# Performance work log

Measured on AMD Instinct MI355X. Metric: run time of the kernel, lower is better.

Reference implementation:

```python
import jax, jax.numpy as jnp
import numpy as np

NS, NV = 32, 8                      # scalar / vector multiplicities (32x0e + 8x1o)
N_NODES, N_EDGES = 16384, 131072
NEF, HID = 128, 128                 # edge feature dim, MLP hidden
WN = NS*NS + NV*NS + NS*NV + NV*NV  # 1600 tensor-product weights per edge
D = NS + 3*NV                       # 56 node feature dim
INV_SQRT3 = 1.0/np.sqrt(3.0)        # CG coeff for 1o x 1o -> 0e
PATH_NORM = 1.0/np.sqrt(NS + NV)    # fan-in normalization per output irrep
EPS = 1e-5


def setup_inputs() -> dict:
    key = jax.random.key(0)
    ks = jax.random.split(key, 10)
    node_attr = jax.random.normal(ks[0], (N_NODES, D), jnp.float32)
    edge_index = jax.random.randint(ks[1], (2, N_EDGES), 0, N_NODES, dtype=jnp.int64)
    edge_attr = jax.random.normal(ks[2], (N_EDGES, NEF), jnp.float32)
    edge_sh = jax.random.normal(ks[3], (N_EDGES, 4), jnp.float32)
    W1 = jax.random.normal(ks[4], (NEF, HID), jnp.float32) / np.sqrt(NEF)
    b1 = jnp.zeros((HID,), jnp.float32)
    W2 = jax.random.normal(ks[5], (HID, WN), jnp.float32) / np.sqrt(HID)
    b2 = jnp.zeros((WN,), jnp.float32)
    bn_gamma = jnp.ones((NS + NV,), jnp.float32)   # per-irrep scale (scalars then vectors)
    bn_beta = jnp.zeros((NS,), jnp.float32)        # bias only on scalar irreps
    return dict(node_attr=node_attr, edge_attr=edge_attr, edge_sh=edge_sh,
                W1=W1, b1=b1, W2=W2, b2=b2, bn_gamma=bn_gamma, bn_beta=bn_beta,
                edge_index=edge_index)


def reference(node_attr, edge_attr, edge_sh, W1, b1, W2, b2, bn_gamma, bn_beta, edge_index):
    edge_src, edge_dst = edge_index[0], edge_index[1]

    # per-edge tensor-product weights from edge MLP (dropout=0, eval mode)
    w = jax.nn.relu(edge_attr @ W1 + b1) @ W2 + b2            # [E, WN]
    o0 = NS*NS; o1 = o0 + NV*NS; o2 = o1 + NS*NV
    w_ss = w[:, :o0].reshape(-1, NS, NS)   # 0e x 0e -> 0e
    w_vs = w[:, o0:o1].reshape(-1, NV, NS) # 1o x 1o -> 0e
    w_sv = w[:, o1:o2].reshape(-1, NS, NV) # 0e x 1o -> 1o
    w_vv = w[:, o2:].reshape(-1, NV, NV)   # 1o x 0e -> 1o

    # gather node features onto edges
    x = node_attr[edge_dst]                # [E, D]
    xs = x[:, :NS]                         # [E, NS]
    xv = x[:, NS:].reshape(-1, NV, 3)      # [E, NV, 3]
    ss = edge_sh[:, 0]                     # [E]
    sv = edge_sh[:, 1:4]                   # [E, 3]

    # CG tensor product with per-edge fully-connected weights
    dot_vv = jnp.einsum('eim,em->ei', xv, sv) * INV_SQRT3
    out_s = (jnp.einsum('eij,ei->ej', w_ss, xs) * ss[:, None]
             + jnp.einsum('eij,ei->ej', w_vs, dot_vv)) * PATH_NORM          # [E, NS]
    out_v = (jnp.einsum('eij,ei->ej', w_sv, xs)[:, :, None] * sv[:, None, :]
             + jnp.einsum('eij,eim->ejm', w_vv, xv) * ss[:, None, None]) * PATH_NORM  # [E, NV, 3]
    tp = jnp.concatenate([out_s, out_v.reshape(-1, 3*NV)], axis=-1)         # [E, D]

    # scatter-mean to source nodes
    sums = jax.ops.segment_sum(tp, edge_src, num_segments=N_NODES)
    cnt = jax.ops.segment_sum(jnp.ones((tp.shape[0], 1), tp.dtype), edge_src,
                              num_segments=N_NODES)
    out = sums / jnp.maximum(cnt, 1.0)

    # residual (in/out irreps identical -> zero padding is a no-op)
    out = out + node_attr

    # equivariant batch norm (training-mode batch statistics)
    s = out[:, :NS]
    v = out[:, NS:].reshape(-1, NV, 3)
    s = (s - s.mean(0)) / jnp.sqrt(s.var(0) + EPS) * bn_gamma[:NS] + bn_beta
    vn2 = (v * v).sum(-1).mean(0)                               # [NV] mean squared norm
    v = v / jnp.sqrt(vn2 + EPS)[None, :, None] * bn_gamma[NS:][None, :, None]
    return jnp.concatenate([s, v.reshape(-1, 3*NV)], axis=-1)
```

## Files before the change

kernel.cpp:

```cpp
#include <hip/hip_runtime.h>

typedef short short8 __attribute__((ext_vector_type(8)));
typedef unsigned short us4 __attribute__((ext_vector_type(4)));
typedef float floatx4 __attribute__((ext_vector_type(4)));
typedef unsigned short u16;

#define NN 16384
#define NE 131072
#define NEF_ 128
#define DD 56
#define INV_SQRT3F 0.57735026918962576f
#define PATH_NORMF 0.15811388300841897f

__device__ __forceinline__ float bf2f(u16 u) {
    union { unsigned int i; float f; } v; v.i = ((unsigned int)u) << 16; return v.f;
}
__device__ __forceinline__ u16 f2bf(float f) {
    union { float f; unsigned int i; } v; v.f = f;
    unsigned int r = v.i + 0x7fffu + ((v.i >> 16) & 1u);
    return (u16)(r >> 16);
}

__global__ __launch_bounds__(256) void prep(const float* __restrict__ W1,
                                            const float* __restrict__ W2,
                                            u16* __restrict__ W1f,
                                            u16* __restrict__ W2f,
                                            const int* __restrict__ eidx,
                                            int* __restrict__ deg) {
    int b = blockIdx.x;
    if (b < 864) {
        int i = b * 256 + threadIdx.x;
        if (i < 16384) {
            int cc = i >> 13, kk = (i >> 11) & 3, cg = (i >> 9) & 3;
            int lane = (i >> 3) & 63, j = i & 7;
            int q = lane >> 4, m = lane & 15;
            W1f[i] = f2bf(W1[(kk * 32 + q * 8 + j) * 128 + cc * 64 + cg * 16 + m]);
        } else {
            int f = i - 16384;
            int c = f >> 13, kk = (f >> 11) & 3, cg = (f >> 9) & 3;
            int lane = (f >> 3) & 63, j = f & 7;
            int q = lane >> 4, m = lane & 15;
            W2f[f] = f2bf(W2[(kk * 32 + q * 8 + j) * 1600 + c * 64 + cg * 16 + m]);
        }
    } else {
        int e = (b - 864) * 256 + threadIdx.x;
        atomicAdd(&deg[eidx[e]], 1);
    }
}

__global__ __launch_bounds__(1024) void deg_scan(const int* __restrict__ deg,
                                                 int* __restrict__ row_start,
                                                 int* __restrict__ cursor) {
    __shared__ int part[1024];
    const int t = threadIdx.x;
    const int base = t * 16;
    int loc[16];
    int s = 0;
    #pragma unroll
    for (int i = 0; i < 16; i++) { loc[i] = s; s += deg[base + i]; }
    part[t] = s;
    __syncthreads();
    for (int off = 1; off < 1024; off <<= 1) {
        int v = (t >= off) ? part[t - off] : 0;
        __syncthreads();
        part[t] += v;
        __syncthreads();
    }
    int pre = (t == 0) ? 0 : part[t - 1];
    #pragma unroll
    for (int i = 0; i < 16; i++) {
        int v = pre + loc[i];
        row_start[base + i] = v;
        cursor[base + i] = v;
    }
    if (t == 1023) row_start[16384] = pre + s;
}

__global__ __launch_bounds__(256) void edge_scatter(const int* __restrict__ eidx,
                                                    int* __restrict__ cursor,
                                                    int* __restrict__ edge_order) {
    int e = blockIdx.x * 256 + threadIdx.x;
    int p = atomicAdd(&cursor[eidx[e]], 1);
    edge_order[p] = e;
}

__global__ __launch_bounds__(256, 2) void tpconv(
    const float* __restrict__ node_attr, const float* __restrict__ edge_attr,
    const float* __restrict__ edge_sh, const u16* __restrict__ W1f,
    const float* __restrict__ b1, const u16* __restrict__ W2f,
    const float* __restrict__ b2, const int* __restrict__ eidx,
    const int* __restrict__ edge_order,
    float* __restrict__ tp)
{
    __shared__ __align__(16) char smem[42496];
    u16*   sA  = (u16*)smem;
    u16*   sF  = (u16*)(smem + 17408);
    float* b2s = (float*)(smem + 26112);
    float* Ssc  = (float*)smem;
    float* Svec = (float*)(smem + 16896);

    const int t = threadIdx.x;
    const int lane = t & 63;
    const int cg = t >> 6;
    const int m = lane & 15;
    const int q = lane >> 4;
    const int p0 = blockIdx.x * 64;

    short8 fc[4];
    #pragma unroll
    for (int kk = 0; kk < 4; kk++)
        fc[kk] = *(const short8*)&W2f[(kk * 4 + cg) * 512 + lane * 8];

    for (int i = t; i < 1600; i += 256) b2s[i] = b2[i];

    #pragma unroll
    for (int ii = 0; ii < 8; ii++) {
        int cid = t + 256 * ii;
        int r = cid >> 5, s = cid & 31;
        int e = edge_order[p0 + r];
        const float* src = &edge_attr[(size_t)e * NEF_ + s * 4];
        us4 o;
        o.x = f2bf(src[0]); o.y = f2bf(src[1]); o.z = f2bf(src[2]); o.w = f2bf(src[3]);
        *(us4*)&sA[r * 136 + s * 4] = o;
    }
    {
        int e = t & 63, p = t >> 6;
        int eg = edge_order[p0 + e];
        int nd = eidx[NE + eg];
        const float* na = node_attr + (size_t)nd * DD;
        const float* sh = edge_sh + (size_t)eg * 4;
        if (p < 2) {
            #pragma unroll
            for (int k = 0; k < 16; k++)
                sF[(p * 16 + k) * 64 + e] = f2bf(na[p * 16 + k]);
        } else {
            #pragma unroll
            for (int k = 0; k < 12; k++)
                sF[(40 + (p - 2) * 12 + k) * 64 + e] = f2bf(na[32 + (p - 2) * 12 + k]);
        }
        sF[(64 + p) * 64 + e] = f2bf(sh[p]);
        float s0 = sh[1], s1 = sh[2], s2 = sh[3];
        #pragma unroll
        for (int s = 0; s < 2; s++) {
            int i = p + 4 * s;
            float d = (na[32 + 3 * i] * s0 + na[33 + 3 * i] * s1 + na[34 + 3 * i] * s2) * INV_SQRT3F;
            sF[(32 + i) * 64 + e] = f2bf(d);
        }
    }
    __syncthreads();

    floatx4 hacc[2][4];
    #pragma unroll
    for (int cc = 0; cc < 2; cc++) {
        short8 g[4];
        #pragma unroll
        for (int kk = 0; kk < 4; kk++)
            g[kk] = *(const short8*)&W1f[cc * 8192 + (kk * 4 + cg) * 512 + lane * 8];
        float bv = b1[cc * 64 + cg * 16 + m];
        #pragma unroll
        for (int et = 0; et < 4; et++) hacc[cc][et] = (floatx4){bv, bv, bv, bv};
        #pragma unroll
        for (int kk = 0; kk < 4; kk++)
            #pragma unroll
            for (int et = 0; et < 4; et++) {
                short8 a = *(const short8*)&sA[(et * 16 + m) * 136 + kk * 32 + q * 8];
                hacc[cc][et] = __builtin_amdgcn_mfma_f32_16x16x32_bf16(a, g[kk], hacc[cc][et], 0, 0, 0);
            }
    }
    __syncthreads();
    #pragma unroll
    for (int cc = 0; cc < 2; cc++)
      #pragma unroll
      for (int et = 0; et < 4; et++)
        #pragma unroll
        for (int r = 0; r < 4; r++) {
            int e = et * 16 + q * 4 + r;
            float v = hacc[cc][et][r];
            sA[e * 136 + cc * 64 + cg * 16 + m] = f2bf(v > 0.f ? v : 0.f);
        }
    __syncthreads();

    short8 hc[4][4];
    #pragma unroll
    for (int et = 0; et < 4; et++)
        #pragma unroll
        for (int kk = 0; kk < 4; kk++)
            hc[et][kk] = *(const short8*)&sA[(et * 16 + m) * 136 + kk * 32 + q * 8];

    float ssc[4], svc[4][3];
    #pragma unroll
    for (int et = 0; et < 4; et++) {
        ssc[et]    = bf2f(sF[64 * 64 + et * 16 + m]);
        svc[et][0] = bf2f(sF[65 * 64 + et * 16 + m]);
        svc[et][1] = bf2f(sF[66 * 64 + et * 16 + m]);
        svc[et][2] = bf2f(sF[67 * 64 + et * 16 + m]);
    }

    float tps[4][4];
    float tpv[4][4][3];
    #pragma unroll
    for (int et = 0; et < 4; et++)
        #pragma unroll
        for (int r = 0; r < 4; r++) {
            tps[et][r] = 0.f;
            tpv[et][r][0] = 0.f; tpv[et][r][1] = 0.f; tpv[et][r][2] = 0.f;
        }

    short8 fn[4];
    for (int c = 0; c < 25; c++) {
        if (c < 24) {
            #pragma unroll
            for (int kk = 0; kk < 4; kk++)
                fn[kk] = *(const short8*)&W2f[(size_t)(c + 1) * 8192 + (kk * 4 + cg) * 512 + lane * 8];
        }
        floatx4 bias = *(const floatx4*)&b2s[c * 64 + cg * 16 + q * 4];
        floatx4 acc[4];
        #pragma unroll
        for (int et = 0; et < 4; et++) acc[et] = bias;
        #pragma unroll
        for (int kk = 0; kk < 4; kk++)
            #pragma unroll
            for (int et = 0; et < 4; et++)
                acc[et] = __builtin_amdgcn_mfma_f32_16x16x32_bf16(fc[kk], hc[et][kk], acc[et], 0, 0, 0);

        if (c < 16) {
            const int i = 2 * c + (cg >> 1);
            #pragma unroll
            for (int et = 0; et < 4; et++) {
                float f = bf2f(sF[i * 64 + et * 16 + m]) * ssc[et];
                #pragma unroll
                for (int r = 0; r < 4; r++) tps[et][r] += acc[et][r] * f;
            }
        } else if (c < 20) {
            const int i = 2 * (c - 16) + (cg >> 1);
            #pragma unroll
            for (int et = 0; et < 4; et++) {
                float f = bf2f(sF[(32 + i) * 64 + et * 16 + m]);
                #pragma unroll
                for (int r = 0; r < 4; r++) tps[et][r] += acc[et][r] * f;
            }
        } else if (c < 24) {
            const int i = 8 * (c - 20) + cg * 2 + (q >> 1);
            #pragma unroll
            for (int et = 0; et < 4; et++) {
                float f = bf2f(sF[i * 64 + et * 16 + m]);
                #pragma unroll
                for (int r = 0; r < 4; r++) {
                    float t0 = acc[et][r] * f;
                    tpv[et][r][0] += t0 * svc[et][0];
                    tpv[et][r][1] += t0 * svc[et][1];
                    tpv[et][r][2] += t0 * svc[et][2];
                }
            }
        } else {
            const int i = cg * 2 + (q >> 1);
            #pragma unroll
            for (int et = 0; et < 4; et++) {
                float x0 = bf2f(sF[(40 + 3 * i + 0) * 64 + et * 16 + m]) * ssc[et];
                float x1 = bf2f(sF[(40 + 3 * i + 1) * 64 + et * 16 + m]) * ssc[et];
                float x2 = bf2f(sF[(40 + 3 * i + 2) * 64 + et * 16 + m]) * ssc[et];
                #pragma unroll
                for (int r = 0; r < 4; r++) {
                    tpv[et][r][0] += acc[et][r] * x0;
                    tpv[et][r][1] += acc[et][r] * x1;
                    tpv[et][r][2] += acc[et][r] * x2;
                }
            }
        }

        if (c < 24) {
            #pragma unroll
            for (int kk = 0; kk < 4; kk++) fc[kk] = fn[kk];
        }
    }

    __syncthreads();
    #pragma unroll
    for (int et = 0; et < 4; et++)
        #pragma unroll
        for (int r = 0; r < 4; r++)
            Ssc[(cg >> 1) * 2112 + (et * 16 + m) * 33 + (cg & 1) * 16 + q * 4 + r] = tps[et][r];
    #pragma unroll
    for (int et = 0; et < 4; et++)
        #pragma unroll
        for (int r = 0; r < 4; r++)
            #pragma unroll
            for (int mm = 0; mm < 3; mm++) {
                float v = tpv[et][r][mm];
                v += __shfl_xor(v, 32, 64);
                if (q < 2)
                    Svec[cg * 1600 + (et * 16 + m) * 25 + ((q & 1) * 4 + r) * 3 + mm] = v;
            }
    __syncthreads();

    for (int idx = t; idx < 3584; idx += 256) {
        int e = idx / 56, d = idx - e * 56;
        float v;
        if (d < 32) {
            v = Ssc[e * 33 + d] + Ssc[2112 + e * 33 + d];
        } else {
            int dd = d - 32;
            v = Svec[e * 25 + dd] + Svec[1600 + e * 25 + dd]
              + Svec[3200 + e * 25 + dd] + Svec[4800 + e * 25 + dd];
        }
        tp[(size_t)(p0 + e) * DD + d] = v * PATH_NORMF;
    }
}

__global__ __launch_bounds__(256) void gather_finalize(
    const float* __restrict__ tp, const int* __restrict__ row_start,
    const float* __restrict__ node_attr,
    float* __restrict__ ybuf, float* __restrict__ partial)
{
    __shared__ float ps[4][72];
    const int wv = threadIdx.x >> 6, lane = threadIdx.x & 63;
    const int n = blockIdx.x * 4 + wv;
    const int beg = row_start[n], end = row_start[n + 1];
    if (lane < 56) {
        float acc = 0.f;
        for (int p = beg; p < end; p++)
            acc += tp[(size_t)p * DD + lane];
        float inv = 1.f / fmaxf((float)(end - beg), 1.f);
        float y = acc * inv + node_attr[(size_t)n * DD + lane];
        ybuf[(size_t)n * DD + lane] = y;
        if (lane < 32) {
            ps[wv][lane] = y;
            ps[wv][32 + lane] = y * y;
        } else {
            float vv = y * y;
            float v1 = __shfl_down(vv, 1, 64);
            float v2 = __shfl_down(vv, 2, 64);
            int l3 = lane - 32;
            if (l3 % 3 == 0) ps[wv][64 + l3 / 3] = vv + v1 + v2;
        }
    }
    __syncthreads();
    const int t = threadIdx.x;
    if (t < 72)
        partial[(size_t)blockIdx.x * 72 + t] = ps[0][t] + ps[1][t] + ps[2][t] + ps[3][t];
}

__global__ __launch_bounds__(256) void bn_reduce(const float* __restrict__ partial,
                                                 float* __restrict__ stats)
{
    __shared__ float red[256];
    const int d = blockIdx.x;
    const int t = threadIdx.x;
    float a = 0.f;
    for (int i = t; i < 4096; i += 256) a += partial[(size_t)i * 72 + d];
    red[t] = a;
    __syncthreads();
    for (int off = 128; off > 0; off >>= 1) {
        if (t < off) red[t] += red[t + off];
        __syncthreads();
    }
    if (t == 0) stats[d] = red[0] * (1.f / 16384.f);
}

__global__ __launch_bounds__(256) void bn_apply(
    const float* __restrict__ ybuf, const float* __restrict__ stats,
    const float* __restrict__ gamma, const float* __restrict__ beta,
    float* __restrict__ out)
{
    const int i = blockIdx.x * 256 + threadIdx.x;
    const int n = i / 56;
    const int d = i - n * 56;
    float y = ybuf[i];
    float o;
    if (d < 32) {
        float mn  = stats[d];
        float var = stats[32 + d] - mn * mn;
        o = (y - mn) * rsqrtf(var + 1e-5f) * gamma[d] + beta[d];
    } else {
        int jv = (d - 32) / 3;
        o = y * rsqrtf(stats[64 + jv] + 1e-5f) * gamma[32 + jv];
    }
    out[i] = o;
}

extern "C" void kernel_launch(void* const* d_in, const int* in_sizes, int n_in,
                              void* d_out, int out_size, void* d_ws, size_t ws_size,
                              hipStream_t stream)
{
    const float* node_attr = (const float*)d_in[0];
    const float* edge_attr = (const float*)d_in[1];
    const float* edge_sh   = (const float*)d_in[2];
    const float* W1        = (const float*)d_in[3];
    const float* b1        = (const float*)d_in[4];
    const float* W2        = (const float*)d_in[5];
    const float* b2        = (const float*)d_in[6];
    const float* gamma     = (const float*)d_in[7];
    const float* beta      = (const float*)d_in[8];
    const int*   eidx      = (const int*)d_in[9];

    char* ws = (char*)d_ws;
    u16*   W1f        = (u16*)(ws);
    u16*   W2f        = (u16*)(ws + 32768);
    int*   deg        = (int*)(ws + 442368);
    int*   row_start  = (int*)(ws + 507904);
    int*   cursor     = (int*)(ws + 573696);
    int*   edge_order = (int*)(ws + 639232);
    float* stats      = (float*)(ws + 1163520);
    float* partial    = (float*)(ws + 1164032);
    float* tp         = (float*)(ws + 2343680);
    float* ybuf       = (float*)(ws + 31703808);

    (void)hipMemsetAsync(deg, 0, 65536, stream);
    hipLaunchKernelGGL(prep,            dim3(1376), dim3(256),  0, stream,
                       W1, W2, W1f, W2f, eidx, deg);
    hipLaunchKernelGGL(deg_scan,        dim3(1),    dim3(1024), 0, stream, deg, row_start, cursor);
    hipLaunchKernelGGL(edge_scatter,    dim3(512),  dim3(256),  0, stream, eidx, cursor, edge_order);
    hipLaunchKernelGGL(tpconv,          dim3(2048), dim3(256),  0, stream,
                       node_attr, edge_attr, edge_sh, W1f, b1, W2f, b2, eidx, edge_order, tp);
    hipLaunchKernelGGL(gather_finalize, dim3(4096), dim3(256),  0, stream,
                       tp, row_start, node_attr, ybuf, partial);
    hipLaunchKernelGGL(bn_reduce,       dim3(72),   dim3(256),  0, stream, partial, stats);
    hipLaunchKernelGGL(bn_apply,        dim3(3584), dim3(256),  0, stream,
                       ybuf, stats, gamma, beta, (float*)d_out);
}
```

Baseline: 280.8 us.

## Restructure tpconv to 512 threads with LDS double-buffered W2 and swizzled tiles

The tensor-product kernel now runs 512 threads per block. Each wave owns one 16-edge tile and a 16-column half of each weight chunk, instead of every wave holding all 64 edges in registers. W2 fragments are staged through a double-buffered LDS area and prefetched from global memory one step ahead. The edge-attribute and hidden tiles use an XOR-swizzled LDS layout to avoid bank conflicts, shared memory shrinks, and the scalar outputs are written directly to global memory. The goal is lower register pressure and higher occupancy, at the cost of a barrier on each of the 50 chunk iterations.

```diff
diff --git a/kernel.cpp b/kernel.cpp
--- a/kernel.cpp
+++ b/kernel.cpp
@@ -19,6 +19,10 @@
     union { float f; unsigned int i; } v; v.f = f;
     unsigned int r = v.i + 0x7fffu + ((v.i >> 16) & 1u);
     return (u16)(r >> 16);
+}
+
+__device__ __forceinline__ int sa_off(int row, int col) {
+    return (row << 7) + (col ^ ((row & 7) << 3));
 }
 
 __global__ __launch_bounds__(256) void prep(const float* __restrict__ W1,
@@ -84,7 +88,7 @@
     edge_order[p] = e;
 }
 
-__global__ __launch_bounds__(256, 2) void tpconv(
+__global__ __launch_bounds__(512, 6) void tpconv(
     const float* __restrict__ node_attr, const float* __restrict__ edge_attr,
     const float* __restrict__ edge_sh, const u16* __restrict__ W1f,
     const float* __restrict__ b1, const u16* __restrict__ W2f,
@@ -92,218 +96,192 @@
     const int* __restrict__ edge_order,
     float* __restrict__ tp)
 {
-    __shared__ __align__(16) char smem[42496];
+    __shared__ __align__(16) char smem[32768];
     u16*   sA  = (u16*)smem;
-    u16*   sF  = (u16*)(smem + 17408);
-    float* b2s = (float*)(smem + 26112);
-    float* Ssc  = (float*)smem;
-    float* Svec = (float*)(smem + 16896);
+    u16*   B2a = (u16*)(smem + 16384);
+    u16*   B2b = (u16*)smem;
+    u16*   sF  = (u16*)(smem + 24576);
+    float* Svec = (float*)smem;
 
     const int t = threadIdx.x;
     const int lane = t & 63;
-    const int cg = t >> 6;
+    const int wv = t >> 6;
     const int m = lane & 15;
     const int q = lane >> 4;
+    const int cg = wv & 1;
+    const int eh = wv >> 1;
     const int p0 = blockIdx.x * 64;
 
-    short8 fc[4];
+    const int w2t = (t >> 7) * 2048 + (t & 127) * 8;
+
+    short8 pre = *(const short8*)&W2f[w2t];
+    short8 g[4];
     #pragma unroll
     for (int kk = 0; kk < 4; kk++)
-        fc[kk] = *(const short8*)&W2f[(kk * 4 + cg) * 512 + lane * 8];
-
-    for (int i = t; i < 1600; i += 256) b2s[i] = b2[i];
-
-    #pragma unroll
-    for (int ii = 0; ii < 8; ii++) {
-        int cid = t + 256 * ii;
+        g[kk] = *(const short8*)&W1f[(wv >> 2) * 8192 + (kk * 4 + (wv & 3)) * 512 + lane * 8];
+
+    #pragma unroll
+    for (int ii = 0; ii < 4; ii++) {
+        int cid = t + 512 * ii;
         int r = cid >> 5, s = cid & 31;
         int e = edge_order[p0 + r];
         const float* src = &edge_attr[(size_t)e * NEF_ + s * 4];
         us4 o;
         o.x = f2bf(src[0]); o.y = f2bf(src[1]); o.z = f2bf(src[2]); o.w = f2bf(src[3]);
-        *(us4*)&sA[r * 136 + s * 4] = o;
+        *(us4*)&sA[sa_off(r, s * 4)] = o;
     }
     {
         int e = t & 63, p = t >> 6;
         int eg = edge_order[p0 + e];
         int nd = eidx[NE + eg];
         const float* na = node_attr + (size_t)nd * DD;
-        const float* sh = edge_sh + (size_t)eg * 4;
-        if (p < 2) {
-            #pragma unroll
-            for (int k = 0; k < 16; k++)
-                sF[(p * 16 + k) * 64 + e] = f2bf(na[p * 16 + k]);
-        } else {
-            #pragma unroll
-            for (int k = 0; k < 12; k++)
-                sF[(40 + (p - 2) * 12 + k) * 64 + e] = f2bf(na[32 + (p - 2) * 12 + k]);
-        }
-        sF[(64 + p) * 64 + e] = f2bf(sh[p]);
-        float s0 = sh[1], s1 = sh[2], s2 = sh[3];
-        #pragma unroll
-        for (int s = 0; s < 2; s++) {
-            int i = p + 4 * s;
-            float d = (na[32 + 3 * i] * s0 + na[33 + 3 * i] * s1 + na[34 + 3 * i] * s2) * INV_SQRT3F;
-            sF[(32 + i) * 64 + e] = f2bf(d);
-        }
-    }
-    __syncthreads();
-
-    floatx4 hacc[2][4];
-    #pragma unroll
-    for (int cc = 0; cc < 2; cc++) {
-        short8 g[4];
-        #pragma unroll
-        for (int kk = 0; kk < 4; kk++)
-            g[kk] = *(const short8*)&W1f[cc * 8192 + (kk * 4 + cg) * 512 + lane * 8];
-        float bv = b1[cc * 64 + cg * 16 + m];
-        #pragma unroll
-        for (int et = 0; et < 4; et++) hacc[cc][et] = (floatx4){bv, bv, bv, bv};
-        #pragma unroll
-        for (int kk = 0; kk < 4; kk++)
-            #pragma unroll
-            for (int et = 0; et < 4; et++) {
-                short8 a = *(const short8*)&sA[(et * 16 + m) * 136 + kk * 32 + q * 8];
-                hacc[cc][et] = __builtin_amdgcn_mfma_f32_16x16x32_bf16(a, g[kk], hacc[cc][et], 0, 0, 0);
-            }
-    }
-    __syncthreads();
-    #pragma unroll
-    for (int cc = 0; cc < 2; cc++)
-      #pragma unroll
-      for (int et = 0; et < 4; et++)
-        #pragma unroll
-        for (int r = 0; r < 4; r++) {
-            int e = et * 16 + q * 4 + r;
-            float v = hacc[cc][et][r];
-            sA[e * 136 + cc * 64 + cg * 16 + m] = f2bf(v > 0.f ? v : 0.f);
-        }
-    __syncthreads();
-
-    short8 hc[4][4];
-    #pragma unroll
-    for (int et = 0; et < 4; et++)
-        #pragma unroll
-        for (int kk = 0; kk < 4; kk++)
-            hc[et][kk] = *(const short8*)&sA[(et * 16 + m) * 136 + kk * 32 + q * 8];
-
-    float ssc[4], svc[4][3];
-    #pragma unroll
-    for (int et = 0; et < 4; et++) {
-        ssc[et]    = bf2f(sF[64 * 64 + et * 16 + m]);
-        svc[et][0] = bf2f(sF[65 * 64 + et * 16 + m]);
-        svc[et][1] = bf2f(sF[66 * 64 + et * 16 + m]);
-        svc[et][2] = bf2f(sF[67 * 64 + et * 16 + m]);
-    }
-
-    float tps[4][4];
-    float tpv[4][4][3];
-    #pragma unroll
-    for (int et = 0; et < 4; et++)
-        #pragma unroll
-        for (int r = 0; r < 4; r++) {
-            tps[et][r] = 0.f;
-            tpv[et][r][0] = 0.f; tpv[et][r][1] = 0.f; tpv[et][r][2] = 0.f;
-        }
-
-    short8 fn[4];
-    for (int c = 0; c < 25; c++) {
-        if (c < 24) {
-            #pragma unroll
-            for (int kk = 0; kk < 4; kk++)
-                fn[kk] = *(const short8*)&W2f[(size_t)(c + 1) * 8192 + (kk * 4 + cg) * 512 + lane * 8];
-        }
-        floatx4 bias = *(const floatx4*)&b2s[c * 64 + cg * 16 + q * 4];
-        floatx4 acc[4];
-        #pragma unroll
-        for (int et = 0; et < 4; et++) acc[et] = bias;
-        #pragma unroll
-        for (int kk = 0; kk < 4; kk++)
-            #pragma unroll
-            for (int et = 0; et < 4; et++)
-                acc[et] = __builtin_amdgcn_mfma_f32_16x16x32_bf16(fc[kk], hc[et][kk], acc[et], 0, 0, 0);
-
-        if (c < 16) {
-            const int i = 2 * c + (cg >> 1);
-            #pragma unroll
-            for (int et = 0; et < 4; et++) {
-                float f = bf2f(sF[i * 64 + et * 16 + m]) * ssc[et];
-                #pragma unroll
-                for (int r = 0; r < 4; r++) tps[et][r] += acc[et][r] * f;
-            }
-        } else if (c < 20) {
-            const int i = 2 * (c - 16) + (cg >> 1);
-            #pragma unroll
-            for (int et = 0; et < 4; et++) {
-                float f = bf2f(sF[(32 + i) * 64 + et * 16 + m]);
-                #pragma unroll
-                for (int r = 0; r < 4; r++) tps[et][r] += acc[et][r] * f;
-            }
-        } else if (c < 24) {
-            const int i = 8 * (c - 20) + cg * 2 + (q >> 1);
-            #pragma unroll
-            for (int et = 0; et < 4; et++) {
-                float f = bf2f(sF[i * 64 + et * 16 + m]);
-                #pragma unroll
-                for (int r = 0; r < 4; r++) {
-                    float t0 = acc[et][r] * f;
-                    tpv[et][r][0] += t0 * svc[et][0];
-                    tpv[et][r][1] += t0 * svc[et][1];
-                    tpv[et][r][2] += t0 * svc[et][2];
-                }
+        if (p < 4) {
+            #pragma unroll
+            for (int k = 0; k < 8; k++)
+                sF[(p * 8 + k) * 64 + e] = f2bf(na[p * 8 + k]);
+        } else if (p == 4) {
+            const float* sh = edge_sh + (size_t)eg * 4;
+            float s0 = sh[1], s1 = sh[2], s2 = sh[3];
+            #pragma unroll
+            for (int i = 0; i < 8; i++) {
+                float d = (na[32 + 3 * i] * s0 + na[33 + 3 * i] * s1 + na[34 + 3 * i] * s2) * INV_SQRT3F;
+                sF[(32 + i) * 64 + e] = f2bf(d);
             }
         } else {
-            const int i = cg * 2 + (q >> 1);
-            #pragma unroll
-            for (int et = 0; et < 4; et++) {
-                float x0 = bf2f(sF[(40 + 3 * i + 0) * 64 + et * 16 + m]) * ssc[et];
-                float x1 = bf2f(sF[(40 + 3 * i + 1) * 64 + et * 16 + m]) * ssc[et];
-                float x2 = bf2f(sF[(40 + 3 * i + 2) * 64 + et * 16 + m]) * ssc[et];
-                #pragma unroll
-                for (int r = 0; r < 4; r++) {
-                    tpv[et][r][0] += acc[et][r] * x0;
-                    tpv[et][r][1] += acc[et][r] * x1;
-                    tpv[et][r][2] += acc[et][r] * x2;
-                }
+            #pragma unroll
+            for (int k = 0; k < 8; k++)
+                sF[(40 + (p - 5) * 8 + k) * 64 + e] = f2bf(na[32 + (p - 5) * 8 + k]);
+        }
+    }
+    *(short8*)&B2a[t * 8] = pre;
+    pre = *(const short8*)&W2f[1024 + w2t];
+    __syncthreads();
+
+    floatx4 hacc[4];
+    {
+        float bv = b1[wv * 16 + m];
+        #pragma unroll
+        for (int rt = 0; rt < 4; rt++) hacc[rt] = (floatx4){bv, bv, bv, bv};
+    }
+    #pragma unroll
+    for (int kk = 0; kk < 4; kk++)
+        #pragma unroll
+        for (int rt = 0; rt < 4; rt++) {
+            short8 a = *(const short8*)&sA[sa_off(rt * 16 + m, kk * 32 + q * 8)];
+            hacc[rt] = __builtin_amdgcn_mfma_f32_16x16x32_bf16(a, g[kk], hacc[rt], 0, 0, 0);
+        }
+    __syncthreads();
+    #pragma unroll
+    for (int rt = 0; rt < 4; rt++)
+        #pragma unroll
+        for (int r = 0; r < 4; r++) {
+            int e = rt * 16 + q * 4 + r;
+            float v = hacc[rt][r];
+            sA[sa_off(e, wv * 16 + m)] = f2bf(v > 0.f ? v : 0.f);
+        }
+    __syncthreads();
+
+    short8 hc[4];
+    #pragma unroll
+    for (int kk = 0; kk < 4; kk++)
+        hc[kk] = *(const short8*)&sA[sa_off(eh * 16 + m, kk * 32 + q * 8)];
+
+    float ssc, svc0, svc1, svc2;
+    {
+        int eg = edge_order[p0 + eh * 16 + m];
+        const float* sh = edge_sh + (size_t)eg * 4;
+        ssc = sh[0]; svc0 = sh[1]; svc1 = sh[2]; svc2 = sh[3];
+    }
+    floatx4 bias = *(const floatx4*)&b2[cg * 16 + q * 4];
+
+    __syncthreads();
+
+    float tps[4] = {0.f, 0.f, 0.f, 0.f};
+    float tpv[4][3];
+    #pragma unroll
+    for (int r = 0; r < 4; r++) { tpv[r][0] = 0.f; tpv[r][1] = 0.f; tpv[r][2] = 0.f; }
+
+    const int e = eh * 16 + m;
+
+    #pragma unroll 2
+    for (int c = 0; c < 50; c++) {
+        const u16* rb = (c & 1) ? B2b : B2a;
+        u16*       wb = (c & 1) ? B2a : B2b;
+
+        floatx4 acc = bias;
+        #pragma unroll
+        for (int kk = 0; kk < 4; kk++) {
+            short8 a = *(const short8*)&rb[kk * 1024 + cg * 512 + lane * 8];
+            acc = __builtin_amdgcn_mfma_f32_16x16x32_bf16(a, hc[kk], acc, 0, 0, 0);
+        }
+
+        if (c < 49) {
+            *(short8*)&wb[t * 8] = pre;
+            bias = *(const floatx4*)&b2[(c + 1) * 32 + cg * 16 + q * 4];
+            if (c < 48)
+                pre = *(const short8*)&W2f[(size_t)((c + 2) >> 1) * 8192
+                                           + (size_t)(((c + 2) & 1)) * 1024 + w2t];
+        }
+
+        if (c < 32) {
+            float f = bf2f(sF[c * 64 + e]) * ssc;
+            #pragma unroll
+            for (int r = 0; r < 4; r++) tps[r] += acc[r] * f;
+        } else if (c < 40) {
+            float f = bf2f(sF[c * 64 + e]);
+            #pragma unroll
+            for (int r = 0; r < 4; r++) tps[r] += acc[r] * f;
+        } else if (c < 48) {
+            const int i = 4 * (c - 40) + cg * 2 + (q >> 1);
+            float f = bf2f(sF[i * 64 + e]);
+            #pragma unroll
+            for (int r = 0; r < 4; r++) {
+                float t0 = acc[r] * f;
+                tpv[r][0] += t0 * svc0;
+                tpv[r][1] += t0 * svc1;
+                tpv[r][2] += t0 * svc2;
             }
-        }
-
-        if (c < 24) {
-            #pragma unroll
-            for (int kk = 0; kk < 4; kk++) fc[kk] = fn[kk];
-        }
-    }
-
-    __syncthreads();
-    #pragma unroll
-    for (int et = 0; et < 4; et++)
-        #pragma unroll
-        for (int r = 0; r < 4; r++)
-            Ssc[(cg >> 1) * 2112 + (et * 16 + m) * 33 + (cg & 1) * 16 + q * 4 + r] = tps[et][r];
-    #pragma unroll
-    for (int et = 0; et < 4; et++)
-        #pragma unroll
-        for (int r = 0; r < 4; r++)
-            #pragma unroll
-            for (int mm = 0; mm < 3; mm++) {
-                float v = tpv[et][r][mm];
-                v += __shfl_xor(v, 32, 64);
-                if (q < 2)
-                    Svec[cg * 1600 + (et * 16 + m) * 25 + ((q & 1) * 4 + r) * 3 + mm] = v;
+        } else {
+            const int i = 4 * (c - 48) + cg * 2 + (q >> 1);
+            float x0 = bf2f(sF[(40 + 3 * i    ) * 64 + e]) * ssc;
+            float x1 = bf2f(sF[(40 + 3 * i + 1) * 64 + e]) * ssc;
+            float x2 = bf2f(sF[(40 + 3 * i + 2) * 64 + e]) * ssc;
+            #pragma unroll
+            for (int r = 0; r < 4; r++) {
+                tpv[r][0] += acc[r] * x0;
+                tpv[r][1] += acc[r] * x1;
+                tpv[r][2] += acc[r] * x2;
             }
-    __syncthreads();
-
-    for (int idx = t; idx < 3584; idx += 256) {
-        int e = idx / 56, d = idx - e * 56;
-        float v;
-        if (d < 32) {
-            v = Ssc[e * 33 + d] + Ssc[2112 + e * 33 + d];
-        } else {
-            int dd = d - 32;
-            v = Svec[e * 25 + dd] + Svec[1600 + e * 25 + dd]
-              + Svec[3200 + e * 25 + dd] + Svec[4800 + e * 25 + dd];
-        }
-        tp[(size_t)(p0 + e) * DD + d] = v * PATH_NORMF;
+        }
+
+        __syncthreads();
+    }
+
+    {
+        floatx4 o;
+        o.x = tps[0] * PATH_NORMF; o.y = tps[1] * PATH_NORMF;
+        o.z = tps[2] * PATH_NORMF; o.w = tps[3] * PATH_NORMF;
+        *(floatx4*)&tp[(size_t)(p0 + e) * DD + cg * 16 + q * 4] = o;
+    }
+    #pragma unroll
+    for (int r = 0; r < 4; r++)
+        #pragma unroll
+        for (int mm = 0; mm < 3; mm++) {
+            float v = tpv[r][mm];
+            v += __shfl_xor(v, 32, 64);
+            if (q < 2)
+                Svec[cg * 1600 + e * 25 + (q * 4 + r) * 3 + mm] = v;
+        }
+    __syncthreads();
+
+    {
+        int ee = t >> 3, j0 = (t & 7) * 3;
+        float* dst = &tp[(size_t)(p0 + ee) * DD + 32 + j0];
+        #pragma unroll
+        for (int k = 0; k < 3; k++) {
+            float v = Svec[ee * 25 + j0 + k] + Svec[1600 + ee * 25 + j0 + k];
+            dst[k] = v * PATH_NORMF;
+        }
     }
 }
 
@@ -410,7 +388,7 @@
                        W1, W2, W1f, W2f, eidx, deg);
     hipLaunchKernelGGL(deg_scan,        dim3(1),    dim3(1024), 0, stream, deg, row_start, cursor);
     hipLaunchKernelGGL(edge_scatter,    dim3(512),  dim3(256),  0, stream, eidx, cursor, edge_order);
-    hipLaunchKernelGGL(tpconv,          dim3(2048), dim3(256),  0, stream,
+    hipLaunchKernelGGL(tpconv,          dim3(2048), dim3(512),  0, stream,
                        node_attr, edge_attr, edge_sh, W1f, b1, W2f, b2, eidx, edge_order, tp);
     hipLaunchKernelGGL(gather_finalize, dim3(4096), dim3(256),  0, stream,
                        tp, row_start, node_attr, ybuf, partial);
```

Measured after the change: 283.1 us. No clear change (+0.8%).
